# Kernel optimization log

Measured on AMD Instinct MI355X. Metric: run time of the kernel, lower is better.

Reference implementation:

```python
import jax, jax.numpy as jnp
import numpy as np
import math

EMBED_DIM = 128
NUM_HEADS = 8
TANH_CLIP = 10.0
L, N, S, E = 1, 1024, 2000, 128


def setup_inputs() -> dict:
    key = jax.random.key(0)
    ks = jax.random.split(key, 7)
    query = jax.random.normal(ks[0], (L, N, E), dtype=jnp.float32)
    glimpse_K = jax.random.normal(ks[1], (S, N, E), dtype=jnp.float32)
    glimpse_V = jax.random.normal(ks[2], (S, N, E), dtype=jnp.float32)
    logit_K = jax.random.normal(ks[3], (N, S, E), dtype=jnp.float32)
    attn_mask = jax.random.randint(ks[4], (N, L, S), 0, 2).astype(jnp.bool_)
    # glimpse_proj params (nn.Linear: y = x @ W.T + b)
    lim = 1.0 / math.sqrt(E)
    W = jax.random.uniform(ks[5], (E, E), dtype=jnp.float32, minval=-lim, maxval=lim)
    b = jax.random.uniform(ks[6], (E,), dtype=jnp.float32, minval=-lim, maxval=lim)
    return {"query": query, "glimpse_K": glimpse_K, "glimpse_V": glimpse_V,
            "logit_K": logit_K, "attn_mask": attn_mask, "W": W, "b": b}


def reference(query, glimpse_K, glimpse_V, logit_K, attn_mask, W, b):
    H = NUM_HEADS
    tgt_len, bsz, embed_dim = query.shape
    src_len = glimpse_K.shape[0]
    head_dim = embed_dim // H
    neg_min = jnp.finfo(query.dtype).min

    # (L,N,E) -> (H,N,L,hd)
    gQ = query.reshape(tgt_len, bsz, H, head_dim).transpose(2, 1, 0, 3)
    gK = glimpse_K.reshape(src_len, bsz, H, head_dim).transpose(2, 1, 0, 3)
    gV = glimpse_V.reshape(src_len, bsz, H, head_dim).transpose(2, 1, 0, 3)

    # compatibility: (H,N,L,S)
    comp = jnp.einsum('hnld,hnsd->hnls', gQ, gK) / math.sqrt(head_dim)
    comp = jnp.where(attn_mask[None], neg_min, comp)  # broadcast mask over heads

    heads = jnp.einsum('hnls,hnsd->hnld', jax.nn.softmax(comp, axis=-1), gV)
    # (H,N,L,hd) -> (N,L,E)
    glimpse = heads.transpose(1, 2, 0, 3).reshape(bsz, tgt_len, embed_dim)
    final_Q = glimpse @ W.T + b

    logits = jnp.einsum('nle,nse->nls', final_Q, logit_K) / math.sqrt(embed_dim)
    logits = jnp.tanh(logits) * TANH_CLIP
    logits = jnp.where(attn_mask, neg_min, logits)
    log_prob = jax.nn.log_softmax(logits, axis=-1)  # (N,L,S)
    return log_prob.squeeze(1)
```

## Files before the change

### kernel.cpp

```cpp
#include <hip/hip_runtime.h>
#include <cfloat>
#include <math.h>

#define NB      1024
#define SLEN    2000
#define EDIM    128
#define NWAVES  4
#define NSTREAM (NWAVES * 2)
#define SENT    (-1e30f)
#define MASKED_OUT (-3.3895313892515355e38f)

__global__ __launch_bounds__(256, 4)
void attn_decoder_kernel(const float* __restrict__ query,
                         const float* __restrict__ gK,
                         const float* __restrict__ gV,
                         const float* __restrict__ lK,
                         const unsigned char* __restrict__ mask,
                         const float* __restrict__ W,
                         const float* __restrict__ bias,
                         float* __restrict__ out)
{
    const int n    = blockIdx.x;
    const int tid  = threadIdx.x;
    const int wave = tid >> 6;
    const int lane = tid & 63;
    const int half = lane >> 5;
    const int l5   = lane & 31;

    __shared__ float sm[NSTREAM][8];
    __shared__ float sl[NSTREAM][8];
    __shared__ float sacc[NSTREAM][EDIM];
    __shared__ float glimpse[EDIM];
    __shared__ float finalQ[EDIM];
    __shared__ float logits_sh[SLEN];
    __shared__ unsigned char mask_sh[SLEN];
    __shared__ unsigned short idx_sh[SLEN];
    __shared__ float smB[NSTREAM], slB[NSTREAM];
    __shared__ int wave_tot[NWAVES];

    for (int i = tid; i < SLEN; i += 256)
        mask_sh[i] = mask[(size_t)n * SLEN + i];

    const float4 q4 = ((const float4*)(query + (size_t)n * EDIM))[l5];

    __syncthreads();

    int mycnt = 0;
    const int s0c = tid * 8;
    #pragma unroll
    for (int k = 0; k < 8; ++k) {
        const int s = s0c + k;
        if (s < SLEN && !mask_sh[s]) mycnt++;
    }
    int inc = mycnt;
    #pragma unroll
    for (int off = 1; off < 64; off <<= 1) {
        const int v = __shfl_up(inc, off);
        if (lane >= off) inc += v;
    }
    if (lane == 63) wave_tot[wave] = inc;
    __syncthreads();
    int wbase = 0;
    #pragma unroll
    for (int w = 0; w < NWAVES; ++w) if (w < wave) wbase += wave_tot[w];
    const int C = wave_tot[0] + wave_tot[1] + wave_tot[2] + wave_tot[3];
    int pos = wbase + inc - mycnt;
    #pragma unroll
    for (int k = 0; k < 8; ++k) {
        const int s = s0c + k;
        if (s < SLEN && !mask_sh[s]) idx_sh[pos++] = (unsigned short)s;
    }
    __syncthreads();

    const int nIt = (C + 15) >> 4;

    float  mh = SENT, lh = 0.f;
    float4 acc = make_float4(0.f, 0.f, 0.f, 0.f);

    #pragma unroll 1
    for (int it = 0; it < nIt; ++it) {
        const int j0 = it * 16 + wave * 4;
        const int jA = j0 + half;
        const int jB = j0 + 2 + half;
        const bool pA = jA < C;
        const bool pB = jB < C;
        const int sA = idx_sh[pA ? jA : 0];
        const int sB = idx_sh[pB ? jB : 0];
        const size_t offA = ((size_t)sA * NB + n) * EDIM + l5 * 4;
        const size_t offB = ((size_t)sB * NB + n) * EDIM + l5 * 4;
        const float4 kA = *(const float4*)(gK + offA);
        const float4 vA = *(const float4*)(gV + offA);
        const float4 kB = *(const float4*)(gK + offB);
        const float4 vB = *(const float4*)(gV + offB);

        {
            float d = fmaf(q4.x, kA.x, fmaf(q4.y, kA.y, fmaf(q4.z, kA.z, q4.w * kA.w)));
            d += __shfl_xor(d, 1);
            d += __shfl_xor(d, 2);
            const float comp = pA ? d * 0.25f : SENT;
            const float mn = fmaxf(mh, comp);
            const float scale = __expf(mh - mn);
            const float p     = __expf(comp - mn);
            lh = fmaf(lh, scale, p);
            acc.x = fmaf(acc.x, scale, p * vA.x);
            acc.y = fmaf(acc.y, scale, p * vA.y);
            acc.z = fmaf(acc.z, scale, p * vA.z);
            acc.w = fmaf(acc.w, scale, p * vA.w);
            mh = mn;
        }
        {
            float d = fmaf(q4.x, kB.x, fmaf(q4.y, kB.y, fmaf(q4.z, kB.z, q4.w * kB.w)));
            d += __shfl_xor(d, 1);
            d += __shfl_xor(d, 2);
            const float comp = pB ? d * 0.25f : SENT;
            const float mn = fmaxf(mh, comp);
            const float scale = __expf(mh - mn);
            const float p     = __expf(comp - mn);
            lh = fmaf(lh, scale, p);
            acc.x = fmaf(acc.x, scale, p * vB.x);
            acc.y = fmaf(acc.y, scale, p * vB.y);
            acc.z = fmaf(acc.z, scale, p * vB.z);
            acc.w = fmaf(acc.w, scale, p * vB.w);
            mh = mn;
        }
    }

    {
        const int st = wave * 2 + half;
        if ((l5 & 3) == 0) { sm[st][l5 >> 2] = mh; sl[st][l5 >> 2] = lh; }
        ((float4*)sacc[st])[l5] = acc;
    }
    __syncthreads();

    if (tid < EDIM) {
        const int hh = tid >> 4;
        float M = sm[0][hh];
        #pragma unroll
        for (int st = 1; st < NSTREAM; ++st) M = fmaxf(M, sm[st][hh]);
        float L = 0.f, a = 0.f;
        #pragma unroll
        for (int st = 0; st < NSTREAM; ++st) {
            const float f = __expf(sm[st][hh] - M);
            L = fmaf(sl[st][hh], f, L);
            a = fmaf(sacc[st][tid], f, a);
        }
        glimpse[tid] = a / fmaxf(L, 1e-30f);
    }
    __syncthreads();

    {
        const int e  = tid & 127;
        const int k0 = (tid >> 7) * 64;
        const float* Wrow = W + (size_t)e * EDIM + k0;
        const float* g = glimpse + k0;
        float sum = 0.f;
        #pragma unroll 16
        for (int k = 0; k < 64; ++k) sum = fmaf(g[k], Wrow[k], sum);
        ((float*)sacc)[tid] = sum;
    }
    __syncthreads();
    if (tid < EDIM)
        finalQ[tid] = ((float*)sacc)[tid] + ((float*)sacc)[tid + 128] + bias[tid];
    __syncthreads();

    const float4 fq4 = ((const float4*)finalQ)[l5];
    float mB = SENT, lB = 0.f;
    const float* lbase = lK + (size_t)n * SLEN * EDIM;

    #pragma unroll 1
    for (int it = 0; it < nIt; ++it) {
        const int j0 = it * 16 + wave * 4;
        const int jA = j0 + half;
        const int jB = j0 + 2 + half;
        const bool pA = jA < C;
        const bool pB = jB < C;
        const int sA = idx_sh[pA ? jA : 0];
        const int sB = idx_sh[pB ? jB : 0];
        const float4 tA = *(const float4*)(lbase + (size_t)sA * EDIM + l5 * 4);
        const float4 tB = *(const float4*)(lbase + (size_t)sB * EDIM + l5 * 4);

        {
            float d = fmaf(fq4.x, tA.x, fmaf(fq4.y, tA.y, fmaf(fq4.z, tA.z, fq4.w * tA.w)));
            d += __shfl_xor(d, 1);
            d += __shfl_xor(d, 2);
            d += __shfl_xor(d, 4);
            d += __shfl_xor(d, 8);
            d += __shfl_xor(d, 16);
            if (pA) {
                const float x = d * 0.08838834764831845f;
                const float e = __expf(-2.f * fabsf(x));
                const float logit = copysignf(10.f * (1.f - e) / (1.f + e), x);
                if (l5 == 0) logits_sh[sA] = logit;
                const float mn = fmaxf(mB, logit);
                lB = fmaf(lB, __expf(mB - mn), __expf(logit - mn));
                mB = mn;
            }
        }
        {
            float d = fmaf(fq4.x, tB.x, fmaf(fq4.y, tB.y, fmaf(fq4.z, tB.z, fq4.w * tB.w)));
            d += __shfl_xor(d, 1);
            d += __shfl_xor(d, 2);
            d += __shfl_xor(d, 4);
            d += __shfl_xor(d, 8);
            d += __shfl_xor(d, 16);
            if (pB) {
                const float x = d * 0.08838834764831845f;
                const float e = __expf(-2.f * fabsf(x));
                const float logit = copysignf(10.f * (1.f - e) / (1.f + e), x);
                if (l5 == 0) logits_sh[sB] = logit;
                const float mn = fmaxf(mB, logit);
                lB = fmaf(lB, __expf(mB - mn), __expf(logit - mn));
                mB = mn;
            }
        }
    }

    {
        const int st = wave * 2 + half;
        if (l5 == 0) { smB[st] = mB; slB[st] = lB; }
    }
    __syncthreads();

    float M = smB[0];
    #pragma unroll
    for (int st = 1; st < NSTREAM; ++st) M = fmaxf(M, smB[st]);
    float L = 0.f;
    #pragma unroll
    for (int st = 0; st < NSTREAM; ++st) L = fmaf(slB[st], __expf(smB[st] - M), L);
    const float lse = (L > 0.f) ? (M + logf(L)) : 0.f;

    float* orow = out + (size_t)n * SLEN;
    for (int i = tid; i < SLEN; i += 256)
        orow[i] = mask_sh[i] ? MASKED_OUT : (logits_sh[i] - lse);
}

extern "C" void kernel_launch(void* const* d_in, const int* in_sizes, int n_in,
                              void* d_out, int out_size, void* d_ws, size_t ws_size,
                              hipStream_t stream) {
    const float*         query = (const float*)d_in[0];
    const float*         gK    = (const float*)d_in[1];
    const float*         gV    = (const float*)d_in[2];
    const float*         lK    = (const float*)d_in[3];
    const unsigned char* mask  = (const unsigned char*)d_in[4];
    const float*         W     = (const float*)d_in[5];
    const float*         bias  = (const float*)d_in[6];
    float*               out   = (float*)d_out;

    attn_decoder_kernel<<<dim3(NB), dim3(256), 0, stream>>>(
        query, gK, gV, lK, mask, W, bias, out);
}
```

Baseline: 485.5 us.

## Double-buffer gathered K/V and logit-K rows with deeper per-wave tiles

Each wave now handles 8 rows per iteration instead of 4, and the loads for the next tile are issued before the current tile is computed, in both the glimpse attention loop and the logit loop. The goal is more memory-level parallelism in this bandwidth-bound gather, so load latency is hidden behind the online-softmax math. The cost is many more live registers (up to 16 float4 buffers), which could lower occupancy under launch_bounds(256,4) or cause spills.

```diff
diff --git a/kernel.cpp b/kernel.cpp
--- a/kernel.cpp
+++ b/kernel.cpp
@@ -7,6 +7,9 @@
 #define EDIM    128
 #define NWAVES  4
 #define NSTREAM (NWAVES * 2)
+#define RPW     8
+#define TILE    (NWAVES * RPW)
+#define NPAIR   (RPW / 2)
 #define SENT    (-1e30f)
 #define MASKED_OUT (-3.3895313892515355e38f)
 
@@ -72,56 +75,62 @@
     }
     __syncthreads();
 
-    const int nIt = (C + 15) >> 4;
+    const int nIt = (C + TILE - 1) / TILE;
 
     float  mh = SENT, lh = 0.f;
     float4 acc = make_float4(0.f, 0.f, 0.f, 0.f);
 
+    float4 ka[NPAIR], va[NPAIR]; int pa[NPAIR];
+    float4 kb[NPAIR], vb[NPAIR]; int pb[NPAIR];
+
+    auto loadA = [&](int it, float4* kk, float4* vv, int* pp) {
+        const int j0 = it * TILE + wave * RPW;
+        #pragma unroll
+        for (int q = 0; q < NPAIR; ++q) {
+            const int j = j0 + q * 2 + half;
+            const int valid = (j < C) ? 1 : 0;
+            const int s = idx_sh[valid ? j : 0];
+            const size_t off = ((size_t)s * NB + n) * EDIM + l5 * 4;
+            kk[q] = *(const float4*)(gK + off);
+            vv[q] = *(const float4*)(gV + off);
+            pp[q] = valid;
+        }
+    };
+
+    loadA(0, ka, va, pa);
+
     #pragma unroll 1
     for (int it = 0; it < nIt; ++it) {
-        const int j0 = it * 16 + wave * 4;
-        const int jA = j0 + half;
-        const int jB = j0 + 2 + half;
-        const bool pA = jA < C;
-        const bool pB = jB < C;
-        const int sA = idx_sh[pA ? jA : 0];
-        const int sB = idx_sh[pB ? jB : 0];
-        const size_t offA = ((size_t)sA * NB + n) * EDIM + l5 * 4;
-        const size_t offB = ((size_t)sB * NB + n) * EDIM + l5 * 4;
-        const float4 kA = *(const float4*)(gK + offA);
-        const float4 vA = *(const float4*)(gV + offA);
-        const float4 kB = *(const float4*)(gK + offB);
-        const float4 vB = *(const float4*)(gV + offB);
-
-        {
-            float d = fmaf(q4.x, kA.x, fmaf(q4.y, kA.y, fmaf(q4.z, kA.z, q4.w * kA.w)));
+        if (it + 1 < nIt) {
+            loadA(it + 1, kb, vb, pb);
+        } else {
+            #pragma unroll
+            for (int q = 0; q < NPAIR; ++q) {
+                kb[q] = make_float4(0.f, 0.f, 0.f, 0.f);
+                vb[q] = make_float4(0.f, 0.f, 0.f, 0.f);
+                pb[q] = 0;
+            }
+        }
+        #pragma unroll
+        for (int q = 0; q < NPAIR; ++q) {
+            float d = fmaf(q4.x, ka[q].x, fmaf(q4.y, ka[q].y,
+                      fmaf(q4.z, ka[q].z, q4.w * ka[q].w)));
             d += __shfl_xor(d, 1);
             d += __shfl_xor(d, 2);
-            const float comp = pA ? d * 0.25f : SENT;
+            const float comp = pa[q] ? d * 0.25f : SENT;
             const float mn = fmaxf(mh, comp);
             const float scale = __expf(mh - mn);
             const float p     = __expf(comp - mn);
             lh = fmaf(lh, scale, p);
-            acc.x = fmaf(acc.x, scale, p * vA.x);
-            acc.y = fmaf(acc.y, scale, p * vA.y);
-            acc.z = fmaf(acc.z, scale, p * vA.z);
-            acc.w = fmaf(acc.w, scale, p * vA.w);
+            acc.x = fmaf(acc.x, scale, p * va[q].x);
+            acc.y = fmaf(acc.y, scale, p * va[q].y);
+            acc.z = fmaf(acc.z, scale, p * va[q].z);
+            acc.w = fmaf(acc.w, scale, p * va[q].w);
             mh = mn;
         }
-        {
-            float d = fmaf(q4.x, kB.x, fmaf(q4.y, kB.y, fmaf(q4.z, kB.z, q4.w * kB.w)));
-            d += __shfl_xor(d, 1);
-            d += __shfl_xor(d, 2);
-            const float comp = pB ? d * 0.25f : SENT;
-            const float mn = fmaxf(mh, comp);
-            const float scale = __expf(mh - mn);
-            const float p     = __expf(comp - mn);
-            lh = fmaf(lh, scale, p);
-            acc.x = fmaf(acc.x, scale, p * vB.x);
-            acc.y = fmaf(acc.y, scale, p * vB.y);
-            acc.z = fmaf(acc.z, scale, p * vB.z);
-            acc.w = fmaf(acc.w, scale, p * vB.w);
-            mh = mn;
+        #pragma unroll
+        for (int q = 0; q < NPAIR; ++q) {
+            ka[q] = kb[q]; va[q] = vb[q]; pa[q] = pb[q];
         }
     }
 
@@ -167,51 +176,57 @@
     float mB = SENT, lB = 0.f;
     const float* lbase = lK + (size_t)n * SLEN * EDIM;
 
+    float4 ta[NPAIR]; int qa[NPAIR], ra[NPAIR];
+    float4 tb[NPAIR]; int qb[NPAIR], rb[NPAIR];
+
+    auto loadB = [&](int it, float4* tt, int* pp, int* rr) {
+        const int j0 = it * TILE + wave * RPW;
+        #pragma unroll
+        for (int q = 0; q < NPAIR; ++q) {
+            const int j = j0 + q * 2 + half;
+            const int valid = (j < C) ? 1 : 0;
+            const int s = idx_sh[valid ? j : 0];
+            tt[q] = *(const float4*)(lbase + (size_t)s * EDIM + l5 * 4);
+            pp[q] = valid;
+            rr[q] = s;
+        }
+    };
+
+    loadB(0, ta, qa, ra);
+
     #pragma unroll 1
     for (int it = 0; it < nIt; ++it) {
-        const int j0 = it * 16 + wave * 4;
-        const int jA = j0 + half;
-        const int jB = j0 + 2 + half;
-        const bool pA = jA < C;
-        const bool pB = jB < C;
-        const int sA = idx_sh[pA ? jA : 0];
-        const int sB = idx_sh[pB ? jB : 0];
-        const float4 tA = *(const float4*)(lbase + (size_t)sA * EDIM + l5 * 4);
-        const float4 tB = *(const float4*)(lbase + (size_t)sB * EDIM + l5 * 4);
-
-        {
-            float d = fmaf(fq4.x, tA.x, fmaf(fq4.y, tA.y, fmaf(fq4.z, tA.z, fq4.w * tA.w)));
+        if (it + 1 < nIt) {
+            loadB(it + 1, tb, qb, rb);
+        } else {
+            #pragma unroll
+            for (int q = 0; q < NPAIR; ++q) {
+                tb[q] = make_float4(0.f, 0.f, 0.f, 0.f);
+                qb[q] = 0; rb[q] = 0;
+            }
+        }
+        #pragma unroll
+        for (int q = 0; q < NPAIR; ++q) {
+            float d = fmaf(fq4.x, ta[q].x, fmaf(fq4.y, ta[q].y,
+                      fmaf(fq4.z, ta[q].z, fq4.w * ta[q].w)));
             d += __shfl_xor(d, 1);
             d += __shfl_xor(d, 2);
             d += __shfl_xor(d, 4);
             d += __shfl_xor(d, 8);
             d += __shfl_xor(d, 16);
-            if (pA) {
+            if (qa[q]) {
                 const float x = d * 0.08838834764831845f;
                 const float e = __expf(-2.f * fabsf(x));
                 const float logit = copysignf(10.f * (1.f - e) / (1.f + e), x);
-                if (l5 == 0) logits_sh[sA] = logit;
+                if (l5 == 0) logits_sh[ra[q]] = logit;
                 const float mn = fmaxf(mB, logit);
                 lB = fmaf(lB, __expf(mB - mn), __expf(logit - mn));
                 mB = mn;
             }
         }
-        {
-            float d = fmaf(fq4.x, tB.x, fmaf(fq4.y, tB.y, fmaf(fq4.z, tB.z, fq4.w * tB.w)));
-            d += __shfl_xor(d, 1);
-            d += __shfl_xor(d, 2);
-            d += __shfl_xor(d, 4);
-            d += __shfl_xor(d, 8);
-            d += __shfl_xor(d, 16);
-            if (pB) {
-                const float x = d * 0.08838834764831845f;
-                const float e = __expf(-2.f * fabsf(x));
-                const float logit = copysignf(10.f * (1.f - e) / (1.f + e), x);
-                if (l5 == 0) logits_sh[sB] = logit;
-                const float mn = fmaxf(mB, logit);
-                lB = fmaf(lB, __expf(mB - mn), __expf(logit - mn));
-                mB = mn;
-            }
+        #pragma unroll
+        for (int q = 0; q < NPAIR; ++q) {
+            ta[q] = tb[q]; qa[q] = qb[q]; ra[q] = rb[q];
         }
     }
 
```

After: 523.2 us. +7.8%, slower.
